# Kernel tuning notes

Hardware: AMD Instinct MI355X
Metric: run time of the kernel (lower is better)

## Reference

```python
import jax, jax.numpy as jnp
import numpy as np
import math
from jax import lax

L = 16
T = 2 ** 14          # hash table size (power of 2 -> uint32 arithmetic is exact mod T)
F_DIM = 2
N_MIN, N_MAX = 16, 512
_B = math.exp((math.log(N_MAX) - math.log(N_MIN)) / (L - 1))
NS = [int(N_MIN * _B ** i) for i in range(L)]
PRIME = np.uint32(2654435761)


def setup_inputs() -> dict:
    key = jax.random.key(0)
    k1, k2 = jax.random.split(key)
    x = jax.random.uniform(k1, (8, 2, 512, 512), dtype=jnp.float32)
    hash_table = jax.random.uniform(k2, (L, T, F_DIM), dtype=jnp.float32) * 2e-4 - 1e-4
    return {"x": x, "hash_table": hash_table}


def reference(x, hash_table):
    b, c, h, w = x.shape
    feats = []
    for i, n in enumerate(NS):
        kh, kw = h // n, w // n
        # max_pool2d(x*n, (kh,kw), stride=1) -> [b, 2, h-kh+1, w-kw+1]
        g = lax.reduce_window(x * n, -jnp.inf, lax.max,
                              (1, 1, kh, kw), (1, 1, 1, 1), 'VALID')
        g = g.astype(jnp.uint32)  # trunc toward zero, values nonneg and small
        # prime-XOR hash; T is a power of two so uint32 wraparound matches int64 math mod T
        idx = (g[:, 0] ^ (g[:, 1] * PRIME)) % np.uint32(T)  # [b, gh, gw]
        f = hash_table[i][idx]                 # gather -> [b, gh, gw, F_DIM]
        f = jnp.transpose(f, (0, 3, 1, 2))     # [b, F_DIM, gh, gw]
        # bilinear upsample (half-pixel centers == align_corners=False)
        f = jax.image.resize(f, (b, F_DIM, h, w), method='bilinear')
        feats.append(f)
    return jnp.concatenate(feats, axis=1)       # [b, L*F_DIM, h, w]
```

## Files before the change

kernel.cpp:

```cpp
#include <hip/hip_runtime.h>
#include <stdint.h>

#define NLVL 16
#define TSIZE 16384
#define HW 512

typedef float vfloat4 __attribute__((ext_vector_type(4)));

__constant__ int c_n[NLVL] = {16,20,25,32,40,50,64,80,101,128,161,203,256,322,406,512};

__device__ __forceinline__ uint32_t pkmax(uint32_t a, uint32_t b) {
    uint32_t r;
    asm("v_pk_max_u16 %0, %1, %2" : "=v"(r) : "v"(a), "v"(b));
    return r;
}

template<int KK, int P, int NE>
__device__ __forceinline__ void winmaxNU(const uint32_t (&e)[NE], uint32_t (&o)[P]) {
    static_assert(NE >= P + KK - 1, "window overrun");
    if constexpr (KK > P) {
        uint32_t sfx[P];
        sfx[P - 1] = e[P - 1];
#pragma unroll
        for (int t = P - 2; t >= 0; --t) sfx[t] = pkmax(e[t], sfx[t + 1]);
        uint32_t run = e[P];
#pragma unroll
        for (int m = P; m <= P + KK - 2; ++m) {
            if (m > P) run = pkmax(run, e[m]);
            const int j = m - KK + 1;
            if (j >= 0 && j < P) o[j] = pkmax(sfx[j], run);
        }
    } else {
#pragma unroll
        for (int i = 0; i < P; ++i) {
            uint32_t m = e[i];
#pragma unroll
            for (int t = 1; t < KK; ++t) m = pkmax(m, e[i + t]);
            o[i] = m;
        }
    }
}

template<int K>
__device__ __forceinline__ void phaseB(const uint32_t* __restrict__ V,
                                       float2* __restrict__ feat,
                                       const float2* __restrict__ tb, const int tid) {
    if (tid < 99) {
        const int i = tid / 3, g = tid % 3;
        constexpr int NE  = 12 + K - 1;
        constexpr int NCH = (NE + 3) >> 2;
        uint32_t f[NCH * 4];
        const uint4* rp = (const uint4*)(V + i * 68 + 12 * g);
#pragma unroll
        for (int cc = 0; cc < NCH; ++cc) {
            const uint4 q = rp[cc];
            f[4*cc] = q.x; f[4*cc+1] = q.y; f[4*cc+2] = q.z; f[4*cc+3] = q.w;
        }
        uint32_t wm[12];
        winmaxNU<K, 12, NCH * 4>(f, wm);
#pragma unroll
        for (int d = 0; d < 12; ++d) {
            const int j = 12 * g + d;
            if (j < 33) {
                const uint32_t m = wm[d];
                const uint32_t idx = ((m & 0xFFFFu) ^ ((m >> 16) * 2654435761u)) & (TSIZE - 1);
                feat[i * 34 + j] = tb[idx];
            }
        }
    }
}

template<int K>
__device__ __forceinline__ void phaseC(const float2* __restrict__ feat,
                                       float* __restrict__ ob,
                                       const int rmin, const int cmin,
                                       const int tx0, const int ty0, const int tid) {
    constexpr int gh = 513 - K;
    constexpr float s = (float)gh * (1.0f / 512.0f);
    const int bty = tid >> 5, btx = tid & 31;
    const int xo = tx0 + btx;
    const float sxf = ((float)xo + 0.5f) * s - 0.5f;
    const float fxf = floorf(sxf);
    const float wx = sxf - fxf;
    const int x0i = (int)fxf;
    const int jx0 = min(max(x0i, 0), gh - 1) - cmin;
    const int jx1 = min(max(x0i + 1, 0), gh - 1) - cmin;
    for (int oy = bty; oy < 32; oy += 8) {
        const int y = ty0 + oy;
        const float syf = ((float)y + 0.5f) * s - 0.5f;
        const float fyf = floorf(syf);
        const float wy = syf - fyf;
        const int y0i = (int)fyf;
        const int iy0 = min(max(y0i, 0), gh - 1) - rmin;
        const int iy1 = min(max(y0i + 1, 0), gh - 1) - rmin;
        const float2 f00 = feat[iy0 * 34 + jx0], f01 = feat[iy0 * 34 + jx1];
        const float2 f10 = feat[iy1 * 34 + jx0], f11 = feat[iy1 * 34 + jx1];
        const float w11 = wy * wx;
        const float w10 = wy - w11;
        const float w01 = wx - w11;
        const float w00 = 1.0f - wy - wx + w11;
        const float c0 = f00.x * w00 + f01.x * w01 + f10.x * w10 + f11.x * w11;
        const float c1 = f00.y * w00 + f01.y * w01 + f10.y * w10 + f11.y * w11;
        const size_t o = (size_t)y * HW + xo;
        __builtin_nontemporal_store(c0, &ob[o]);
        __builtin_nontemporal_store(c1, &ob[o + (size_t)HW * HW]);
    }
}

template<int K1, int K2>
__device__ __forceinline__ void do_pair(
        const int l1, const int l2, const int b, const int tx0, const int ty0,
        const float* __restrict__ x, const float* __restrict__ table,
        float* __restrict__ out, uint32_t* lds) {
    constexpr float s1 = (float)(513 - K1) * (1.0f / 512.0f);
    constexpr float s2 = (float)(513 - K2) * (1.0f / 512.0f);
    const float nf1 = (float)c_n[l1], nf2 = (float)c_n[l2];
    const int tid = threadIdx.x;

    const float* xb0 = x + (size_t)b * 2 * HW * HW;
    const float* xb1 = xb0 + HW * HW;

    uint32_t* V1  = lds;
    uint32_t* V2  = lds + 2244;
    float2*  feat = (float2*)(lds + 4488);

    const int rmin1 = max((int)floorf(((float)ty0 + 0.5f) * s1 - 0.5f), 0);
    const int cmin1 = max((int)floorf(((float)tx0 + 0.5f) * s1 - 0.5f), 0);
    const int rmin2 = max((int)floorf(((float)ty0 + 0.5f) * s2 - 0.5f), 0);
    const int cmin2 = max((int)floorf(((float)tx0 + 0.5f) * s2 - 0.5f), 0);
    const int dr = rmin2 - rmin1;
    const int dc = cmin2 - cmin1;

    {
        const int wv = __builtin_amdgcn_readfirstlane(tid >> 6);
        const int c  = tid & 63;
        const int r0 = 8 * wv;
        const int xx = min(cmin1 + c, HW - 1);
        const int ybase = rmin1 + r0;
        uint32_t eA[K1 + 8], eB[K1 + 8];
#pragma unroll
        for (int t = 0; t < K1 + 8; ++t) {
            const int yy = min(ybase + t, HW - 1);
            const float v0 = (xb0 + yy * HW)[xx];
            const float v1 = (xb1 + yy * HW)[xx];
            eA[t] = (uint32_t)(v0 * nf1) | ((uint32_t)(v1 * nf1) << 16);
            eB[t] = (uint32_t)(v0 * nf2) | ((uint32_t)(v1 * nf2) << 16);
        }
        uint32_t o1[9];
        winmaxNU<K1, 9, K1 + 8>(eA, o1);
        const int vb = r0 * 68 + c;
#pragma unroll
        for (int t = 0; t < 9; ++t) V1[vb + t * 68] = o1[t];

        constexpr int P2 = K1 - K2 + 9;
        uint32_t o2[P2];
        winmaxNU<K2, P2, K1 + 8>(eB, o2);
        const int c2 = c - dc;
#pragma unroll
        for (int j = 0; j < P2; ++j) {
            const int i2 = r0 + j - dr;
            if (i2 >= 0 && i2 <= 32 && c2 >= 0)
                V2[i2 * 68 + c2] = o2[j];
        }
    }
    __syncthreads();

    phaseB<K1>(V1, feat, (const float2*)table + (size_t)l1 * TSIZE, tid);
    __syncthreads();
    phaseC<K1>(feat, out + ((size_t)b * 32 + l1 * 2) * HW * HW, rmin1, cmin1, tx0, ty0, tid);
    __syncthreads();
    phaseB<K2>(V2, feat, (const float2*)table + (size_t)l2 * TSIZE, tid);
    __syncthreads();
    phaseC<K2>(feat, out + ((size_t)b * 32 + l2 * 2) * HW * HW, rmin2, cmin2, tx0, ty0, tid);
}

template<int K>
__device__ __forceinline__ void do_tile(
        const int lvl, const int b, const int tx0, const int ty0,
        const float* __restrict__ x, const float* __restrict__ table,
        float* __restrict__ out, uint32_t* lds) {
    constexpr float s = (float)(513 - K) * (1.0f / 512.0f);
    const float nf = (float)c_n[lvl];
    const int tid = threadIdx.x;
    const float* xb0 = x + (size_t)b * 2 * HW * HW;
    const float* xb1 = xb0 + HW * HW;
    uint32_t* V   = lds;
    float2*  feat = (float2*)(lds + 2244);

    const int rmin = max((int)floorf(((float)ty0 + 0.5f) * s - 0.5f), 0);
    const int cmin = max((int)floorf(((float)tx0 + 0.5f) * s - 0.5f), 0);
    {
        const int wv = __builtin_amdgcn_readfirstlane(tid >> 6);
        const int c  = tid & 63;
        const int r0 = 8 * wv;
        const int xx = min(cmin + c, HW - 1);
        const int ybase = rmin + r0;
        uint32_t e[K + 8];
#pragma unroll
        for (int t = 0; t < K + 8; ++t) {
            const int yy = min(ybase + t, HW - 1);
            const float v0 = (xb0 + yy * HW)[xx];
            const float v1 = (xb1 + yy * HW)[xx];
            e[t] = (uint32_t)(v0 * nf) | ((uint32_t)(v1 * nf) << 16);
        }
        uint32_t o[9];
        winmaxNU<K, 9, K + 8>(e, o);
        const int vb = r0 * 68 + c;
#pragma unroll
        for (int t = 0; t < 9; ++t) V[vb + t * 68] = o[t];
    }
    __syncthreads();
    phaseB<K>(V, feat, (const float2*)table + (size_t)lvl * TSIZE, tid);
    __syncthreads();
    phaseC<K>(feat, out + ((size_t)b * 32 + lvl * 2) * HW * HW, rmin, cmin, tx0, ty0, tid);
}

__device__ __forceinline__ void identity3(
        const int b, const int tx0, const int ty0,
        const float* __restrict__ x, const float* __restrict__ table,
        float* __restrict__ out) {
    const int tid = threadIdx.x;
    const int oy = tid >> 3, xo = tx0 + (tid & 7) * 4;
    const int y = ty0 + oy;
    const float* xb0 = x + (size_t)b * 2 * HW * HW;
    const float* xb1 = xb0 + HW * HW;
    const float4 v0 = *(const float4*)&xb0[y * HW + xo];
    const float4 v1 = *(const float4*)&xb1[y * HW + xo];
    const size_t o = (size_t)y * HW + xo;
#pragma unroll
    for (int li = 0; li < 3; ++li) {
        const int lvl = 13 + li;
        const float nf = (float)c_n[13 + li];
        const float2* tb = (const float2*)table + (size_t)lvl * TSIZE;
        float* ob = out + ((size_t)b * 32 + lvl * 2) * HW * HW;
        const uint32_t i0 = (((uint32_t)(v0.x * nf)) ^ (((uint32_t)(v1.x * nf)) * 2654435761u)) & (TSIZE - 1);
        const uint32_t i1 = (((uint32_t)(v0.y * nf)) ^ (((uint32_t)(v1.y * nf)) * 2654435761u)) & (TSIZE - 1);
        const uint32_t i2 = (((uint32_t)(v0.z * nf)) ^ (((uint32_t)(v1.z * nf)) * 2654435761u)) & (TSIZE - 1);
        const uint32_t i3 = (((uint32_t)(v0.w * nf)) ^ (((uint32_t)(v1.w * nf)) * 2654435761u)) & (TSIZE - 1);
        const float2 f0 = tb[i0], f1 = tb[i1], f2 = tb[i2], f3 = tb[i3];
        const vfloat4 o0 = (vfloat4){f0.x, f1.x, f2.x, f3.x};
        const vfloat4 o1 = (vfloat4){f0.y, f1.y, f2.y, f3.y};
        __builtin_nontemporal_store(o0, (vfloat4*)&ob[o]);
        __builtin_nontemporal_store(o1, (vfloat4*)&ob[o + (size_t)HW * HW]);
    }
}

__global__ __launch_bounds__(256) void fused_kernel(
        const float* __restrict__ x, const float* __restrict__ table,
        float* __restrict__ out) {
    __shared__ __align__(16) uint32_t lds[6732];

    const int bid  = blockIdx.x;
    const int b    = bid & 7;
    const int tile = (bid >> 3) & 255;
    const int grp  = bid >> 11;
    const int tx0  = (tile & 15) * 32;
    const int ty0  = (tile >> 4) * 32;

    switch (grp) {
        case 0: do_pair<32,25>( 0,  1, b, tx0, ty0, x, table, out, lds); break;
        case 1: do_pair<20,16>( 2,  3, b, tx0, ty0, x, table, out, lds); break;
        case 2: do_pair<12,10>( 4,  5, b, tx0, ty0, x, table, out, lds); break;
        case 3: do_pair< 8, 6>( 6,  7, b, tx0, ty0, x, table, out, lds); break;
        case 4: do_pair< 5, 4>( 8,  9, b, tx0, ty0, x, table, out, lds); break;
        case 5: do_pair< 3, 2>(10, 11, b, tx0, ty0, x, table, out, lds); break;
        case 6: do_tile< 2>(12, b, tx0, ty0, x, table, out, lds); break;
        default: identity3(b, tx0, ty0, x, table, out); break;
    }
}

extern "C" void kernel_launch(void* const* d_in, const int* in_sizes, int n_in,
                              void* d_out, int out_size, void* d_ws, size_t ws_size,
                              hipStream_t stream) {
    const float* x     = (const float*)d_in[0];
    const float* table = (const float*)d_in[1];
    float* out         = (float*)d_out;
    (void)d_ws; (void)ws_size;

    fused_kernel<<<dim3(8 * 256 * 8), dim3(256), 0, stream>>>(x, table, out);
}
```

Measured before the change: 106.0 us.

## Process four hash levels per block sharing one column load, pad LDS strides

Each block now handles four pyramid levels instead of two. It loads the input column once as floats and derives all four quantized max-window chains from registers, which cuts redundant global reads of x and reduces the grid from 8 to 5 block groups. The LDS row stride is padded per level so that it is not a multiple of 8, to avoid bank conflicts. The sliding-window max is replaced by a block-wise prefix/suffix van Herk scheme. In exchange, LDS per block grows, register pressure rises, and the work per block becomes less balanced across groups.

```diff
diff --git a/kernel.cpp b/kernel.cpp
--- a/kernel.cpp
+++ b/kernel.cpp
@@ -15,49 +15,78 @@
     return r;
 }
 
+constexpr int padS(int w) {
+    int s = (w + 3) & ~3;
+    if (s % 8 == 0) s += 4;
+    return s;
+}
+
 template<int KK, int P, int NE>
-__device__ __forceinline__ void winmaxNU(const uint32_t (&e)[NE], uint32_t (&o)[P]) {
+__device__ __forceinline__ void winmax(const uint32_t (&e)[NE], uint32_t (&o)[P]) {
     static_assert(NE >= P + KK - 1, "window overrun");
-    if constexpr (KK > P) {
-        uint32_t sfx[P];
-        sfx[P - 1] = e[P - 1];
-#pragma unroll
-        for (int t = P - 2; t >= 0; --t) sfx[t] = pkmax(e[t], sfx[t + 1]);
-        uint32_t run = e[P];
-#pragma unroll
-        for (int m = P; m <= P + KK - 2; ++m) {
-            if (m > P) run = pkmax(run, e[m]);
-            const int j = m - KK + 1;
-            if (j >= 0 && j < P) o[j] = pkmax(sfx[j], run);
-        }
+    if constexpr (KK == 1) {
+#pragma unroll
+        for (int j = 0; j < P; ++j) o[j] = e[j];
     } else {
-#pragma unroll
-        for (int i = 0; i < P; ++i) {
-            uint32_t m = e[i];
-#pragma unroll
-            for (int t = 1; t < KK; ++t) m = pkmax(m, e[i + t]);
-            o[i] = m;
-        }
-    }
-}
-
-template<int K>
+        constexpr int NB = (P + KK - 1) / KK;
+#pragma unroll
+        for (int bb = 0; bb < NB; ++bb) {
+            const int j0 = bb * KK;
+            uint32_t sfx[KK];
+            sfx[KK - 1] = e[j0 + KK - 1];
+#pragma unroll
+            for (int t = KK - 2; t >= 0; --t) sfx[t] = pkmax(e[j0 + t], sfx[t + 1]);
+            o[j0] = sfx[0];
+            uint32_t run = 0;
+#pragma unroll
+            for (int d = 1; d < KK; ++d) {
+                if (j0 + d < P) {
+                    run = (d == 1) ? e[j0 + KK] : pkmax(run, e[j0 + KK + d - 1]);
+                    o[j0 + d] = pkmax(sfx[d], run);
+                }
+            }
+        }
+    }
+}
+
+template<int K1, int Ki, int Si>
+__device__ __forceinline__ void vchain(const float (&v0)[K1 + 8], const float (&v1)[K1 + 8],
+                                       const float nfi, uint32_t* __restrict__ Vi,
+                                       const int c, const int r0,
+                                       const int dri, const int dci) {
+    constexpr int Pi = K1 - Ki + 9;
+    uint32_t e[K1 + 8];
+#pragma unroll
+    for (int t = 0; t < K1 + 8; ++t)
+        e[t] = (uint32_t)(v0[t] * nfi) | ((uint32_t)(v1[t] * nfi) << 16);
+    uint32_t o[Pi];
+    winmax<Ki, Pi, K1 + 8>(e, o);
+    const int ci = c - dci;
+    if (ci >= 0 && ci < Si) {
+#pragma unroll
+        for (int j = 0; j < Pi; ++j) {
+            const int i2 = r0 + j - dri;
+            if (i2 >= 0 && i2 <= 32) Vi[i2 * Si + ci] = o[j];
+        }
+    }
+}
+
+template<int K, int S>
 __device__ __forceinline__ void phaseB(const uint32_t* __restrict__ V,
                                        float2* __restrict__ feat,
                                        const float2* __restrict__ tb, const int tid) {
     if (tid < 99) {
         const int i = tid / 3, g = tid % 3;
-        constexpr int NE  = 12 + K - 1;
-        constexpr int NCH = (NE + 3) >> 2;
+        constexpr int NCH = (K + 14) >> 2;
         uint32_t f[NCH * 4];
-        const uint4* rp = (const uint4*)(V + i * 68 + 12 * g);
+        const uint4* rp = (const uint4*)(V + i * S + 12 * g);
 #pragma unroll
         for (int cc = 0; cc < NCH; ++cc) {
             const uint4 q = rp[cc];
             f[4*cc] = q.x; f[4*cc+1] = q.y; f[4*cc+2] = q.z; f[4*cc+3] = q.w;
         }
         uint32_t wm[12];
-        winmaxNU<K, 12, NCH * 4>(f, wm);
+        winmax<K, 12, NCH * 4>(f, wm);
 #pragma unroll
         for (int d = 0; d < 12; ++d) {
             const int j = 12 * g + d;
@@ -107,29 +136,37 @@
     }
 }
 
-template<int K1, int K2>
-__device__ __forceinline__ void do_pair(
-        const int l1, const int l2, const int b, const int tx0, const int ty0,
+template<int K1, int K2, int K3, int K4>
+__device__ __forceinline__ void do_quad(
+        const int l1, const int l2, const int l3, const int l4,
+        const int b, const int tx0, const int ty0,
         const float* __restrict__ x, const float* __restrict__ table,
         float* __restrict__ out, uint32_t* lds) {
+    constexpr int S1 = padS(32 + K1), S2 = padS(32 + K2);
+    constexpr int S3 = padS(32 + K3), S4 = padS(32 + K4);
     constexpr float s1 = (float)(513 - K1) * (1.0f / 512.0f);
     constexpr float s2 = (float)(513 - K2) * (1.0f / 512.0f);
-    const float nf1 = (float)c_n[l1], nf2 = (float)c_n[l2];
+    constexpr float s3 = (float)(513 - K3) * (1.0f / 512.0f);
+    constexpr float s4 = (float)(513 - K4) * (1.0f / 512.0f);
     const int tid = threadIdx.x;
+
+    uint32_t* V1 = lds;
+    uint32_t* V2 = V1 + 33 * S1;
+    uint32_t* V3 = V2 + 33 * S2;
+    uint32_t* V4 = V3 + 33 * S3;
+    float2*  feat = (float2*)(V4 + 33 * S4);
 
     const float* xb0 = x + (size_t)b * 2 * HW * HW;
     const float* xb1 = xb0 + HW * HW;
-
-    uint32_t* V1  = lds;
-    uint32_t* V2  = lds + 2244;
-    float2*  feat = (float2*)(lds + 4488);
 
     const int rmin1 = max((int)floorf(((float)ty0 + 0.5f) * s1 - 0.5f), 0);
     const int cmin1 = max((int)floorf(((float)tx0 + 0.5f) * s1 - 0.5f), 0);
     const int rmin2 = max((int)floorf(((float)ty0 + 0.5f) * s2 - 0.5f), 0);
     const int cmin2 = max((int)floorf(((float)tx0 + 0.5f) * s2 - 0.5f), 0);
-    const int dr = rmin2 - rmin1;
-    const int dc = cmin2 - cmin1;
+    const int rmin3 = max((int)floorf(((float)ty0 + 0.5f) * s3 - 0.5f), 0);
+    const int cmin3 = max((int)floorf(((float)tx0 + 0.5f) * s3 - 0.5f), 0);
+    const int rmin4 = max((int)floorf(((float)ty0 + 0.5f) * s4 - 0.5f), 0);
+    const int cmin4 = max((int)floorf(((float)tx0 + 0.5f) * s4 - 0.5f), 0);
 
     {
         const int wv = __builtin_amdgcn_readfirstlane(tid >> 6);
@@ -137,41 +174,35 @@
         const int r0 = 8 * wv;
         const int xx = min(cmin1 + c, HW - 1);
         const int ybase = rmin1 + r0;
-        uint32_t eA[K1 + 8], eB[K1 + 8];
+        float v0[K1 + 8], v1[K1 + 8];
 #pragma unroll
         for (int t = 0; t < K1 + 8; ++t) {
             const int yy = min(ybase + t, HW - 1);
-            const float v0 = (xb0 + yy * HW)[xx];
-            const float v1 = (xb1 + yy * HW)[xx];
-            eA[t] = (uint32_t)(v0 * nf1) | ((uint32_t)(v1 * nf1) << 16);
-            eB[t] = (uint32_t)(v0 * nf2) | ((uint32_t)(v1 * nf2) << 16);
-        }
-        uint32_t o1[9];
-        winmaxNU<K1, 9, K1 + 8>(eA, o1);
-        const int vb = r0 * 68 + c;
-#pragma unroll
-        for (int t = 0; t < 9; ++t) V1[vb + t * 68] = o1[t];
-
-        constexpr int P2 = K1 - K2 + 9;
-        uint32_t o2[P2];
-        winmaxNU<K2, P2, K1 + 8>(eB, o2);
-        const int c2 = c - dc;
-#pragma unroll
-        for (int j = 0; j < P2; ++j) {
-            const int i2 = r0 + j - dr;
-            if (i2 >= 0 && i2 <= 32 && c2 >= 0)
-                V2[i2 * 68 + c2] = o2[j];
-        }
-    }
-    __syncthreads();
-
-    phaseB<K1>(V1, feat, (const float2*)table + (size_t)l1 * TSIZE, tid);
+            v0[t] = (xb0 + yy * HW)[xx];
+            v1[t] = (xb1 + yy * HW)[xx];
+        }
+        vchain<K1, K1, S1>(v0, v1, (float)c_n[l1], V1, c, r0, 0, 0);
+        vchain<K1, K2, S2>(v0, v1, (float)c_n[l2], V2, c, r0, rmin2 - rmin1, cmin2 - cmin1);
+        vchain<K1, K3, S3>(v0, v1, (float)c_n[l3], V3, c, r0, rmin3 - rmin1, cmin3 - cmin1);
+        vchain<K1, K4, S4>(v0, v1, (float)c_n[l4], V4, c, r0, rmin4 - rmin1, cmin4 - cmin1);
+    }
+    __syncthreads();
+
+    phaseB<K1, S1>(V1, feat, (const float2*)table + (size_t)l1 * TSIZE, tid);
     __syncthreads();
     phaseC<K1>(feat, out + ((size_t)b * 32 + l1 * 2) * HW * HW, rmin1, cmin1, tx0, ty0, tid);
     __syncthreads();
-    phaseB<K2>(V2, feat, (const float2*)table + (size_t)l2 * TSIZE, tid);
+    phaseB<K2, S2>(V2, feat, (const float2*)table + (size_t)l2 * TSIZE, tid);
     __syncthreads();
     phaseC<K2>(feat, out + ((size_t)b * 32 + l2 * 2) * HW * HW, rmin2, cmin2, tx0, ty0, tid);
+    __syncthreads();
+    phaseB<K3, S3>(V3, feat, (const float2*)table + (size_t)l3 * TSIZE, tid);
+    __syncthreads();
+    phaseC<K3>(feat, out + ((size_t)b * 32 + l3 * 2) * HW * HW, rmin3, cmin3, tx0, ty0, tid);
+    __syncthreads();
+    phaseB<K4, S4>(V4, feat, (const float2*)table + (size_t)l4 * TSIZE, tid);
+    __syncthreads();
+    phaseC<K4>(feat, out + ((size_t)b * 32 + l4 * 2) * HW * HW, rmin4, cmin4, tx0, ty0, tid);
 }
 
 template<int K>
@@ -179,13 +210,14 @@
         const int lvl, const int b, const int tx0, const int ty0,
         const float* __restrict__ x, const float* __restrict__ table,
         float* __restrict__ out, uint32_t* lds) {
+    constexpr int S = padS(32 + K);
     constexpr float s = (float)(513 - K) * (1.0f / 512.0f);
     const float nf = (float)c_n[lvl];
     const int tid = threadIdx.x;
     const float* xb0 = x + (size_t)b * 2 * HW * HW;
     const float* xb1 = xb0 + HW * HW;
     uint32_t* V   = lds;
-    float2*  feat = (float2*)(lds + 2244);
+    float2*  feat = (float2*)(lds + 33 * S);
 
     const int rmin = max((int)floorf(((float)ty0 + 0.5f) * s - 0.5f), 0);
     const int cmin = max((int)floorf(((float)tx0 + 0.5f) * s - 0.5f), 0);
@@ -195,22 +227,17 @@
         const int r0 = 8 * wv;
         const int xx = min(cmin + c, HW - 1);
         const int ybase = rmin + r0;
-        uint32_t e[K + 8];
+        float v0[K + 8], v1[K + 8];
 #pragma unroll
         for (int t = 0; t < K + 8; ++t) {
             const int yy = min(ybase + t, HW - 1);
-            const float v0 = (xb0 + yy * HW)[xx];
-            const float v1 = (xb1 + yy * HW)[xx];
-            e[t] = (uint32_t)(v0 * nf) | ((uint32_t)(v1 * nf) << 16);
-        }
-        uint32_t o[9];
-        winmaxNU<K, 9, K + 8>(e, o);
-        const int vb = r0 * 68 + c;
-#pragma unroll
-        for (int t = 0; t < 9; ++t) V[vb + t * 68] = o[t];
-    }
-    __syncthreads();
-    phaseB<K>(V, feat, (const float2*)table + (size_t)lvl * TSIZE, tid);
+            v0[t] = (xb0 + yy * HW)[xx];
+            v1[t] = (xb1 + yy * HW)[xx];
+        }
+        vchain<K, K, S>(v0, v1, nf, V, c, r0, 0, 0);
+    }
+    __syncthreads();
+    phaseB<K, S>(V, feat, (const float2*)table + (size_t)lvl * TSIZE, tid);
     __syncthreads();
     phaseC<K>(feat, out + ((size_t)b * 32 + lvl * 2) * HW * HW, rmin, cmin, tx0, ty0, tid);
 }
@@ -248,7 +275,7 @@
 __global__ __launch_bounds__(256) void fused_kernel(
         const float* __restrict__ x, const float* __restrict__ table,
         float* __restrict__ out) {
-    __shared__ __align__(16) uint32_t lds[6732];
+    __shared__ __align__(16) uint32_t lds[9900];
 
     const int bid  = blockIdx.x;
     const int b    = bid & 7;
@@ -258,13 +285,10 @@
     const int ty0  = (tile >> 4) * 32;
 
     switch (grp) {
-        case 0: do_pair<32,25>( 0,  1, b, tx0, ty0, x, table, out, lds); break;
-        case 1: do_pair<20,16>( 2,  3, b, tx0, ty0, x, table, out, lds); break;
-        case 2: do_pair<12,10>( 4,  5, b, tx0, ty0, x, table, out, lds); break;
-        case 3: do_pair< 8, 6>( 6,  7, b, tx0, ty0, x, table, out, lds); break;
-        case 4: do_pair< 5, 4>( 8,  9, b, tx0, ty0, x, table, out, lds); break;
-        case 5: do_pair< 3, 2>(10, 11, b, tx0, ty0, x, table, out, lds); break;
-        case 6: do_tile< 2>(12, b, tx0, ty0, x, table, out, lds); break;
+        case 0: do_quad<32,25,20,16>( 0,  1,  2,  3, b, tx0, ty0, x, table, out, lds); break;
+        case 1: do_quad<12,10, 8, 6>( 4,  5,  6,  7, b, tx0, ty0, x, table, out, lds); break;
+        case 2: do_quad< 5, 4, 3, 2>( 8,  9, 10, 11, b, tx0, ty0, x, table, out, lds); break;
+        case 3: do_tile<2>(12, b, tx0, ty0, x, table, out, lds); break;
         default: identity3(b, tx0, ty0, x, table, out); break;
     }
 }
@@ -277,5 +301,5 @@
     float* out         = (float*)d_out;
     (void)d_ws; (void)ws_size;
 
-    fused_kernel<<<dim3(8 * 256 * 8), dim3(256), 0, stream>>>(x, table, out);
-}
+    fused_kernel<<<dim3(5 * 256 * 8), dim3(256), 0, stream>>>(x, table, out);
+}
```

New measurement: 115.7 us. 9.1% more time.
